# Kernel optimization log

Measured on AMD Instinct MI355X. Metric: run time of the kernel, lower is better.

The kernel has to match this reference:

```python
import jax, jax.numpy as jnp
import numpy as np

MIN_NORM = 1e-15
BALL_EPS = 1e-5  # proj margin, c = 1
HYPER_BETA = 1.0


def _artanh(x):
    x = jnp.clip(x, -1.0 + 1e-7, 1.0 - 1e-7)
    return jnp.arctanh(x)


def _proj(x):
    # clip points inside the unit Poincare ball
    norm = jnp.maximum(jnp.linalg.norm(x, axis=-1, keepdims=True), MIN_NORM)
    maxnorm = 1.0 - BALL_EPS
    return jnp.where(norm > maxnorm, x / norm * maxnorm, x)


def _expmap0(u):
    un = jnp.maximum(jnp.linalg.norm(u, axis=-1, keepdims=True), MIN_NORM)
    return jnp.tanh(un) * u / un


def _mobius_add(x, y):
    x2 = jnp.sum(x * x, axis=-1, keepdims=True)
    y2 = jnp.sum(y * y, axis=-1, keepdims=True)
    xy = jnp.sum(x * y, axis=-1, keepdims=True)
    num = (1.0 + 2.0 * xy + y2) * x + (1.0 - x2) * y
    den = 1.0 + 2.0 * xy + x2 * y2
    return num / jnp.maximum(den, MIN_NORM)


def _sqdist(p, q):
    ma = _mobius_add(-p, q)
    d = 2.0 * _artanh(jnp.linalg.norm(ma, axis=-1))
    return d * d


def _to_klein(x):
    return 2.0 * x / (1.0 + jnp.sum(x * x, axis=-1, keepdims=True))


def _lorentz_factor(x):
    return 1.0 / jnp.sqrt(jnp.maximum(1.0 - jnp.sum(x * x, axis=-1), 1e-7))


def _klein_to(x):
    return x / (1.0 + jnp.sqrt(jnp.maximum(1.0 - jnp.sum(x * x, axis=-1, keepdims=True), 0.0)))


def _logmap0(p):
    pn = jnp.maximum(jnp.linalg.norm(p, axis=-1, keepdims=True), MIN_NORM)
    return _artanh(pn) * p / pn


def setup_inputs() -> dict:
    key = jax.random.key(0)
    k1, k2, k3, k4, k5 = jax.random.split(key, 5)
    B, L, V, D, A, S = 4096, 50, 50000, 200, 14, 30
    inputs = jax.random.randint(k1, (B, L), 0, V, dtype=jnp.int32)
    emb = jax.random.normal(k2, (V, D), dtype=jnp.float32) * 0.1  # w2v * 0.1 as in student_init
    xav = float(np.sqrt(6.0 / (D + D)))
    M = jax.random.uniform(k3, (D, D), dtype=jnp.float32, minval=-xav, maxval=xav)
    a_emb = jax.random.normal(k4, (A, S, D), dtype=jnp.float32) * 0.1
    sw = jax.random.uniform(k5, (A, S), dtype=jnp.float32)
    seed_w = sw / jnp.sum(jnp.abs(sw), axis=1, keepdims=True)  # L1-normalized
    return {"inputs": inputs, "emb": emb, "M": M, "a_emb": a_emb, "seed_w": seed_w}


def reference(inputs, emb, M, a_emb, seed_w):
    # --- AttentionEncoder ---
    x_wrd = emb[inputs]                                   # [B,L,D] gather
    x_avg = jnp.mean(x_wrd, axis=1)                       # [B,D]
    scores = jnp.einsum('bld,de,be->bl', x_wrd, M, x_avg)  # [B,L]
    a = jax.nn.softmax(scores, axis=1)
    enc = jnp.einsum('bl,bld->bd', a, x_wrd)              # [B,D]

    # --- hyperbolic projection ---
    enc = _proj(_expmap0(enc))                            # [B,D] on Poincare ball
    a_emb_w = jnp.sum(a_emb * seed_w[:, :, None], axis=1)  # [A,D]
    hyp_a = _proj(_expmap0(a_emb_w))                      # [A,D]

    sqd = _sqdist(enc[:, None, :], hyp_a[None, :, :])     # [B,A]
    probs_exp = jnp.exp(-HYPER_BETA * sqd - 0.05)         # [B,A]
    a_probs = probs_exp / jnp.sum(probs_exp, axis=1, keepdims=True)

    kle = _to_klein(hyp_a)                                # [A,D]
    lf = _lorentz_factor(kle)                             # [A]
    probs = lf[None, :] * probs_exp                       # [B,A]
    probs_expanded = (probs / jnp.sum(probs, axis=1, keepdims=True))[:, :, None]  # [B,A,1]

    kle_o = jnp.sum(kle[None, :, :] * probs_expanded, axis=1)  # [B,D] Klein barycenter
    r = _klein_to(kle_o)                                  # [B,D]
    eu_r = _logmap0(r)                                    # [B,D]
    return eu_r, probs_expanded, a_probs
```

## Files before the change

### kernel.cpp

```cpp
#include <hip/hip_runtime.h>
#include <hip/hip_fp16.h>
#include <math.h>

#define B_ 4096
#define L_ 50
#define D_ 200
#define A_ 14
#define S_ 30

#define WS_HYP   0
#define WS_KLE   (A_ * D_)
#define WS_Y2    (2 * A_ * D_)
#define WS_LF    (WS_Y2 + A_)
#define WS_MH    8192
#define WS_V     8192

__device__ __forceinline__ float wave_reduce_sum(float v) {
    #pragma unroll
    for (int off = 32; off > 0; off >>= 1) v += __shfl_down(v, off, 64);
    return v;
}
__device__ __forceinline__ float bfly_sum(float v) {
    #pragma unroll
    for (int m = 32; m > 0; m >>= 1) v += __shfl_xor(v, m, 64);
    return v;
}
__device__ __forceinline__ float bfly_sum16(float v) {
    #pragma unroll
    for (int m = 8; m > 0; m >>= 1) v += __shfl_xor(v, m, 64);
    return v;
}
__device__ __forceinline__ float block_reduce_512(float val, volatile float* red) {
    __syncthreads();
    val = wave_reduce_sum(val);
    if ((threadIdx.x & 63) == 0) red[threadIdx.x >> 6] = val;
    __syncthreads();
    float s = 0.f;
    #pragma unroll
    for (int i = 0; i < 8; ++i) s += red[i];
    return s;
}

typedef _Float16 h2v __attribute__((ext_vector_type(2)));
__device__ __forceinline__ float fd2(unsigned a, unsigned b, float c) {
#if __has_builtin(__builtin_amdgcn_fdot2)
    return __builtin_amdgcn_fdot2(__builtin_bit_cast(h2v, a),
                                  __builtin_bit_cast(h2v, b), c, false);
#else
    __half2 ha = __builtin_bit_cast(__half2, a), hb = __builtin_bit_cast(__half2, b);
    float2 fa = __half22float2(ha), fb = __half22float2(hb);
    return fmaf(fa.x, fb.x, fmaf(fa.y, fb.y, c));
#endif
}
__device__ __forceinline__ unsigned packh2(float a, float b) {
    __half2 h = __floats2half2_rn(a, b);
    return __builtin_bit_cast(unsigned, h);
}

__global__ __launch_bounds__(256) void precompute_anchors(
    const float* __restrict__ a_emb, const float* __restrict__ seed_w,
    float* __restrict__ ws)
{
    __shared__ float u[A_][D_];
    __shared__ float nrm2[A_];
    const int t = threadIdx.x;
    const int wave = t >> 6, lane = t & 63;

    for (int d = t; d < D_; d += 256) {
        for (int a = 0; a < A_; ++a) {
            float acc = 0.f;
            #pragma unroll 5
            for (int s = 0; s < S_; ++s)
                acc += a_emb[(a * S_ + s) * D_ + d] * seed_w[a * S_ + s];
            u[a][d] = acc;
        }
    }
    __syncthreads();

    for (int a = wave; a < A_; a += 4) {
        float s = 0.f;
        for (int d = lane; d < D_; d += 64) s += u[a][d] * u[a][d];
        s = wave_reduce_sum(s);
        if (lane == 0) nrm2[a] = s;
    }
    __syncthreads();

    float* hyp = ws + WS_HYP;
    float* kle = ws + WS_KLE;
    float* y2  = ws + WS_Y2;
    float* lf  = ws + WS_LF;
    const float maxn = 1.0f - 1e-5f;

    for (int a = 0; a < A_; ++a) {
        float un = fmaxf(sqrtf(nrm2[a]), 1e-15f);
        float th = tanhf(un);
        float pn = fminf(th, maxn);
        float s  = pn / un;
        float py2 = pn * pn;
        float kscale = 2.0f / (1.0f + py2);
        float k2 = py2 * kscale * kscale;
        if (t == 0) {
            y2[a] = py2;
            lf[a] = 1.0f / sqrtf(fmaxf(1.0f - k2, 1e-7f));
        }
        for (int d = t; d < D_; d += 256) {
            float h = u[a][d] * s;
            hyp[a * D_ + d] = h;
            kle[a * D_ + d] = h * kscale;
        }
    }
}

__global__ __launch_bounds__(256) void convert_M(
    const float* __restrict__ M, __half* __restrict__ Mh)
{
    int i = blockIdx.x * 256 + threadIdx.x;
    if (i < D_ * D_) Mh[i] = __float2half(M[i]);
}

__global__ __launch_bounds__(256, 6) void fused_wave2(
    const int*   __restrict__ inputs,
    const float* __restrict__ emb,
    const float* __restrict__ ws,
    float* __restrict__ out)
{
    __shared__ float xav[2][2][D_];
    __shared__ float vsh[2][D_];
    __shared__ float ench[2][2][D_];
    __shared__ float msh[2][2][2];

    const float*  kle = ws + WS_KLE;
    const float*  y2  = ws + WS_Y2;
    const float*  lf  = ws + WS_LF;
    const __half* Mh  = (const __half*)(ws + WS_MH);

    const int wid  = threadIdx.x >> 6, lane = threadIdx.x & 63;
    const int rib  = wid >> 1;
    const int h    = wid & 1;
    const int b    = blockIdx.x * 2 + rib;
    const bool L50 = (lane < 50);

    const int sidx = inputs[b * L_ + (L50 ? lane : 0)];
    const int off  = L50 ? 4 * lane : 0;
    const int lbase = 25 * h;

    float a0 = 0.f, a1 = 0.f, a2 = 0.f, a3 = 0.f;
    #pragma unroll 5
    for (int j = 0; j < 25; ++j) {
        const int row = __shfl(sidx, lbase + j, 64);
        float4 x = *(const float4*)(emb + (size_t)row * D_ + off);
        a0 += x.x; a1 += x.y; a2 += x.z; a3 += x.w;
    }
    if (L50) {
        xav[rib][h][4 * lane + 0] = a0;
        xav[rib][h][4 * lane + 1] = a1;
        xav[rib][h][4 * lane + 2] = a2;
        xav[rib][h][4 * lane + 3] = a3;
    }
    __syncthreads();
    unsigned xu0 = 0, xu1 = 0;
    if (L50) {
        const float inv = 1.0f / (float)L_;
        float f0 = (xav[rib][0][4 * lane + 0] + xav[rib][1][4 * lane + 0]) * inv;
        float f1 = (xav[rib][0][4 * lane + 1] + xav[rib][1][4 * lane + 1]) * inv;
        float f2 = (xav[rib][0][4 * lane + 2] + xav[rib][1][4 * lane + 2]) * inv;
        float f3 = (xav[rib][0][4 * lane + 3] + xav[rib][1][4 * lane + 3]) * inv;
        xu0 = packh2(f0, f1);
        xu1 = packh2(f2, f3);
    }

    {
        float w0 = 0.f, w1 = 0.f;
        const int mr = 100 * h + 2 * (L50 ? lane : 0);
        const __half* m0 = Mh + (size_t)(mr + 0) * D_;
        const __half* m1 = Mh + (size_t)(mr + 1) * D_;
        #pragma unroll 5
        for (int c = 0; c < 25; ++c) {
            unsigned xa = __shfl(xu0, 2 * c,     64);
            unsigned xb = __shfl(xu1, 2 * c,     64);
            unsigned xc = __shfl(xu0, 2 * c + 1, 64);
            unsigned xd = __shfl(xu1, 2 * c + 1, 64);
            uint4 q0 = *(const uint4*)(m0 + 8 * c);
            uint4 q1 = *(const uint4*)(m1 + 8 * c);
            w0 = fd2(q0.x, xa, w0); w0 = fd2(q0.y, xb, w0); w0 = fd2(q0.z, xc, w0); w0 = fd2(q0.w, xd, w0);
            w1 = fd2(q1.x, xa, w1); w1 = fd2(q1.y, xb, w1); w1 = fd2(q1.z, xc, w1); w1 = fd2(q1.w, xd, w1);
        }
        if (L50) { vsh[rib][mr] = w0; vsh[rib][mr + 1] = w1; }
    }
    __syncthreads();
    float v0 = 0.f, v1 = 0.f, v2 = 0.f, v3 = 0.f;
    if (L50) {
        v0 = vsh[rib][4 * lane + 0];
        v1 = vsh[rib][4 * lane + 1];
        v2 = vsh[rib][4 * lane + 2];
        v3 = vsh[rib][4 * lane + 3];
    }

    float m = -INFINITY, ssum = 0.f;
    float e0 = 0.f, e1 = 0.f, e2 = 0.f, e3 = 0.f;
    {
        float4 bufA[5], bufB[5];
        auto LOADC = [&](float4* xb, int base) {
            #pragma unroll
            for (int j = 0; j < 5; ++j) {
                const int r = __shfl(sidx, lbase + base + j, 64);
                xb[j] = *(const float4*)(emb + (size_t)r * D_ + off);
            }
        };
        auto PROC = [&](const float4* xb) {
            #pragma unroll
            for (int j = 0; j < 5; ++j) {
                const float4 x = xb[j];
                float part = L50 ? (x.x * v0 + x.y * v1 + x.z * v2 + x.w * v3) : 0.f;
                const float s = bfly_sum(part);
                if (s > m) {
                    const float r = expf(m - s);
                    ssum *= r; e0 *= r; e1 *= r; e2 *= r; e3 *= r;
                    m = s;
                }
                const float w = expf(s - m);
                ssum += w;
                e0 = fmaf(w, x.x, e0); e1 = fmaf(w, x.y, e1);
                e2 = fmaf(w, x.z, e2); e3 = fmaf(w, x.w, e3);
            }
        };
        LOADC(bufA, 0);
        LOADC(bufB, 5);  PROC(bufA);
        LOADC(bufA, 10); PROC(bufB);
        LOADC(bufB, 15); PROC(bufA);
        LOADC(bufA, 20); PROC(bufB);
        PROC(bufA);
    }
    if (L50) {
        ench[rib][h][4 * lane + 0] = e0;
        ench[rib][h][4 * lane + 1] = e1;
        ench[rib][h][4 * lane + 2] = e2;
        ench[rib][h][4 * lane + 3] = e3;
    }
    if (lane == 0) { msh[rib][h][0] = m; msh[rib][h][1] = ssum; }
    __syncthreads();

    {
        const float mo  = msh[rib][1 - h][0];
        const float sso = msh[rib][1 - h][1];
        const float M   = fmaxf(m, mo);
        const float wA  = expf(m - M);
        const float wB  = expf(mo - M);
        const float st  = ssum * wA + sso * wB;
        const float rs  = 1.0f / st;
        if (L50) {
            e0 = (e0 * wA + ench[rib][1 - h][4 * lane + 0] * wB) * rs;
            e1 = (e1 * wA + ench[rib][1 - h][4 * lane + 1] * wB) * rs;
            e2 = (e2 * wA + ench[rib][1 - h][4 * lane + 2] * wB) * rs;
            e3 = (e3 * wA + ench[rib][1 - h][4 * lane + 3] * wB) * rs;
        } else {
            e0 = e1 = e2 = e3 = 0.f;
        }
    }

    const float n2 = bfly_sum(e0 * e0 + e1 * e1 + e2 * e2 + e3 * e3);
    const float un = fmaxf(sqrtf(n2), 1e-15f);
    const float pn = fminf(tanhf(un), 1.0f - 1e-5f);
    const float ps = pn / un;
    const float x2 = pn * pn;
    const float p0 = e0 * ps, p1 = e1 * ps, p2 = e2 * ps, p3 = e3 * ps;

    float kd = 0.f;
    #pragma unroll
    for (int a = 0; a < A_; ++a) {
        float4 k = *(const float4*)(kle + a * D_ + off);
        float part = L50 ? (p0 * k.x + p1 * k.y + p2 * k.z + p3 * k.w) : 0.f;
        float d = bfly_sum(part);
        if (lane == a) kd = d;
    }

    float px = 0.f, lfv = 0.f;
    if (lane < A_) {
        const float yy  = y2[lane];
        lfv = lf[lane];
        const float dot = kd * (1.0f + yy) * 0.5f;
        const float c1 = 1.0f - 2.0f * dot + yy;
        const float c2 = 1.0f - x2;
        const float num2 = c1 * c1 * x2 - 2.0f * c1 * c2 * dot + c2 * c2 * yy;
        const float den  = fmaxf(1.0f - 2.0f * dot + x2 * yy, 1e-15f);
        const float nma  = sqrtf(fmaxf(num2, 0.f)) / den;
        const float z    = fminf(nma, 1.0f - 1e-7f);
        const float dist = logf((1.0f + z) / (1.0f - z));
        px = expf(-dist * dist - 0.05f);
    }
    const float se = bfly_sum16(px);
    const float sp = bfly_sum16(lfv * px);
    float pev = 0.f;
    if (lane < A_) {
        pev = lfv * px / sp;
        if (h == 0) {
            out[B_ * D_ + b * A_ + lane] = pev;
            out[B_ * D_ + B_ * A_ + b * A_ + lane] = px / se;
        }
    }

    float k0 = 0.f, k1 = 0.f, k2 = 0.f, k3 = 0.f;
    #pragma unroll
    for (int a = 0; a < A_; ++a) {
        const float w = __shfl(pev, a, 64);
        float4 k = *(const float4*)(kle + a * D_ + off);
        k0 = fmaf(w, k.x, k0); k1 = fmaf(w, k.y, k1);
        k2 = fmaf(w, k.z, k2); k3 = fmaf(w, k.w, k3);
    }
    if (!L50) { k0 = k1 = k2 = k3 = 0.f; }
    const float n2k = bfly_sum(k0 * k0 + k1 * k1 + k2 * k2 + k3 * k3);
    const float denom = 1.0f + sqrtf(fmaxf(1.0f - n2k, 0.f));
    const float r2 = n2k / (denom * denom);
    const float rn = fmaxf(sqrtf(r2), 1e-15f);
    const float z2 = fminf(rn, 1.0f - 1e-7f);
    const float fac = 0.5f * logf((1.0f + z2) / (1.0f - z2)) / rn;
    if (L50 && h == 0) {
        float4 o = make_float4(fac * k0 / denom, fac * k1 / denom,
                               fac * k2 / denom, fac * k3 / denom);
        *(float4*)(out + (size_t)b * D_ + 4 * lane) = o;
    }
}

#define G_R 8
__global__ __launch_bounds__(512) void gather_gemm(
    const int* __restrict__ inputs, const float* __restrict__ emb,
    const float* __restrict__ M, float* __restrict__ ws)
{
    __shared__ __align__(16) float xs[G_R][D_ + 4];
    __shared__ int sidx[G_R][L_];
    float* v = ws + WS_V;
    const int b0 = blockIdx.x * G_R;
    const int t = threadIdx.x;
    const int wave = t >> 6, lane = t & 63;

    for (int p = t; p < G_R * L_; p += 512) sidx[p / L_][p % L_] = inputs[b0 * L_ + p];
    __syncthreads();

    if (lane < D_ / 4) {
        float ax = 0.f, ay = 0.f, az = 0.f, aw = 0.f;
        #pragma unroll
        for (int l = 0; l < L_; ++l) {
            const float4 vv = ((const float4*)(emb + (size_t)sidx[wave][l] * D_))[lane];
            ax += vv.x; ay += vv.y; az += vv.z; aw += vv.w;
        }
        const float inv = 1.0f / (float)L_;
        ((float4*)xs[wave])[lane] = make_float4(ax * inv, ay * inv, az * inv, aw * inv);
    }
    __syncthreads();

    const int r = t & 7, dg = t >> 3;
    const float4* xr4 = (const float4*)xs[r];
    #pragma unroll
    for (int k = 0; k < 4; ++k) {
        const int d = dg + 64 * k;
        if (d < D_) {
            const float4* Mr4 = (const float4*)(M + d * D_);
            float acc = 0.f;
            #pragma unroll
            for (int e = 0; e < D_ / 4; ++e) {
                float4 m4 = Mr4[e], x4 = xr4[e];
                acc += m4.x * x4.x + m4.y * x4.y + m4.z * x4.z + m4.w * x4.w;
            }
            v[(size_t)(b0 + r) * D_ + d] = acc;
        }
    }
}

__global__ __launch_bounds__(512, 8) void fused_main(
    const int*   __restrict__ inputs,
    const float* __restrict__ emb,
    const float* __restrict__ ws,
    float* __restrict__ out)
{
    __shared__ __align__(16) float x[L_][D_];
    __shared__ float attn[L_];
    __shared__ int   sidx[L_];
    __shared__ float red[8];
    __shared__ float sums[2];

    const float* hyp = ws + WS_HYP;
    const float* kle = ws + WS_KLE;
    const float* y2  = ws + WS_Y2;
    const float* lf  = ws + WS_LF;
    const float* vg  = ws + WS_V;

    const int b = blockIdx.x;
    const int t = threadIdx.x;
    const int wave = t >> 6, lane = t & 63;

    float vr0 = vg[(size_t)b * D_ + lane];
    float vr1 = vg[(size_t)b * D_ + lane + 64];
    float vr2 = vg[(size_t)b * D_ + lane + 128];
    float vr3 = (lane < D_ - 192) ? vg[(size_t)b * D_ + lane + 192] : 0.f;

    if (t < L_) sidx[t] = inputs[b * L_ + t];
    __syncthreads();

    {
        const int DQ = D_ / 4;
        const int p0 = t, p1 = t + 512, p2 = t + 1024, p3 = t + 1536, p4 = t + 2048;
        const bool has4 = (p4 < L_ * DQ);
        float4 a0 = ((const float4*)(emb + (size_t)sidx[p0 / DQ] * D_))[p0 % DQ];
        float4 a1 = ((const float4*)(emb + (size_t)sidx[p1 / DQ] * D_))[p1 % DQ];
        float4 a2 = ((const float4*)(emb + (size_t)sidx[p2 / DQ] * D_))[p2 % DQ];
        float4 a3 = ((const float4*)(emb + (size_t)sidx[p3 / DQ] * D_))[p3 % DQ];
        float4 a4;
        if (has4) a4 = ((const float4*)(emb + (size_t)sidx[p4 / DQ] * D_))[p4 % DQ];
        ((float4*)x[p0 / DQ])[p0 % DQ] = a0;
        ((float4*)x[p1 / DQ])[p1 % DQ] = a1;
        ((float4*)x[p2 / DQ])[p2 % DQ] = a2;
        ((float4*)x[p3 / DQ])[p3 % DQ] = a3;
        if (has4) ((float4*)x[p4 / DQ])[p4 % DQ] = a4;
    }
    __syncthreads();

    for (int l = wave; l < L_; l += 8) {
        float s = x[l][lane] * vr0 + x[l][lane + 64] * vr1 + x[l][lane + 128] * vr2;
        if (lane < D_ - 192) s += x[l][lane + 192] * vr3;
        s = wave_reduce_sum(s);
        if (lane == 0) attn[l] = s;
    }
    __syncthreads();

    if (wave == 0) {
        float scv = (lane < L_) ? attn[lane] : -INFINITY;
        float m = scv;
        #pragma unroll
        for (int off = 32; off > 0; off >>= 1) m = fmaxf(m, __shfl_xor(m, off, 64));
        float e = (lane < L_) ? expf(scv - m) : 0.f;
        float ss = e;
        #pragma unroll
        for (int off = 32; off > 0; off >>= 1) ss += __shfl_xor(ss, off, 64);
        if (lane < L_) attn[lane] = e / ss;
    }
    __syncthreads();

    float encv = 0.f;
    if (t < D_) {
        #pragma unroll 10
        for (int l = 0; l < L_; ++l) encv += attn[l] * x[l][t];
    }

    float n2 = block_reduce_512((t < D_) ? encv * encv : 0.f, red);
    const float maxn = 1.0f - 1e-5f;
    float un = fmaxf(sqrtf(n2), 1e-15f);
    float pn = fminf(tanhf(un), maxn);
    float ps = pn / un;
    float x2 = pn * pn;
    float* pvec  = &x[0][0];
    float* dotpq = &x[1][0];
    float* pexp  = &x[1][16];
    float* pe    = &x[1][32];
    if (t < D_) pvec[t] = encv * ps;
    __syncthreads();

    for (int a = wave; a < A_; a += 8) {
        const float* ha = hyp + a * D_;
        float s = ha[lane] * pvec[lane] + ha[lane + 64] * pvec[lane + 64]
                + ha[lane + 128] * pvec[lane + 128];
        if (lane < D_ - 192) s += ha[lane + 192] * pvec[lane + 192];
        s = wave_reduce_sum(s);
        if (lane == 0) dotpq[a] = s;
    }
    __syncthreads();

    if (t < A_) {
        float dot = dotpq[t];
        float yy  = y2[t];
        float c1 = 1.0f - 2.0f * dot + yy;
        float c2 = 1.0f - x2;
        float num2 = c1 * c1 * x2 - 2.0f * c1 * c2 * dot + c2 * c2 * yy;
        float den  = fmaxf(1.0f - 2.0f * dot + x2 * yy, 1e-15f);
        float nma  = sqrtf(fmaxf(num2, 0.f)) / den;
        float z    = fminf(nma, 1.0f - 1e-7f);
        float dist = logf((1.0f + z) / (1.0f - z));
        pexp[t] = expf(-dist * dist - 0.05f);
    }
    __syncthreads();
    if (t == 0) {
        float se = 0.f, sp = 0.f;
        for (int a = 0; a < A_; ++a) { se += pexp[a]; sp += lf[a] * pexp[a]; }
        sums[0] = 1.0f / se;
        sums[1] = 1.0f / sp;
    }
    __syncthreads();
    if (t < A_) {
        float ap  = pexp[t] * sums[0];
        float pev = lf[t] * pexp[t] * sums[1];
        pe[t] = pev;
        out[B_ * D_ + b * A_ + t] = pev;
        out[B_ * D_ + B_ * A_ + b * A_ + t] = ap;
    }
    __syncthreads();

    float ko = 0.f;
    if (t < D_) {
        #pragma unroll
        for (int a = 0; a < A_; ++a) ko += kle[a * D_ + t] * pe[a];
    }
    float n2k = block_reduce_512((t < D_) ? ko * ko : 0.f, red);
    if (t < D_) {
        float denom = 1.0f + sqrtf(fmaxf(1.0f - n2k, 0.f));
        float rv = ko / denom;
        float r2 = n2k / (denom * denom);
        float rn = fmaxf(sqrtf(r2), 1e-15f);
        float z  = fminf(rn, 1.0f - 1e-7f);
        float fac = (0.5f * logf((1.0f + z) / (1.0f - z))) / rn;
        out[b * D_ + t] = fac * rv;
    }
}

extern "C" void kernel_launch(void* const* d_in, const int* in_sizes, int n_in,
                              void* d_out, int out_size, void* d_ws, size_t ws_size,
                              hipStream_t stream) {
    (void)in_sizes; (void)n_in; (void)out_size;
    const int*   inputs = (const int*)  d_in[0];
    const float* emb    = (const float*)d_in[1];
    const float* M      = (const float*)d_in[2];
    const float* a_emb  = (const float*)d_in[3];
    const float* seed_w = (const float*)d_in[4];
    float* out = (float*)d_out;
    float* ws  = (float*)d_ws;

    precompute_anchors<<<1, 256, 0, stream>>>(a_emb, seed_w, ws);

    const size_t need = (size_t)(WS_MH + (D_ * D_ + 1) / 2) * sizeof(float);
    if (ws_size >= need) {
        __half* Mh = (__half*)(ws + WS_MH);
        convert_M<<<(D_ * D_ + 255) / 256, 256, 0, stream>>>(M, Mh);
        fused_wave2<<<B_ / 2, 256, 0, stream>>>(inputs, emb, ws, out);
    } else {
        gather_gemm<<<B_ / G_R, 512, 0, stream>>>(inputs, emb, M, ws);
        fused_main<<<B_, 512, 0, stream>>>(inputs, emb, ws, out);
    }
}
```

Before: 111.2 us.

## Convert embedding table to fp16 and cache gathered rows in registers

Adds a per-call pass that converts the whole 50000x200 embedding table to half precision in workspace. A new fused kernel then gathers half rows, keeps the 25 gathered rows per wave in registers, and reuses them for the mean, the scores and the weighted sum, replacing repeated global reloads. The conversion pass reads 40MB and writes 20MB on every call, which may cost more than the gather traffic it saves. Embeddings are also rounded to fp16, which adds numerical error.

```diff
diff --git a/kernel.cpp b/kernel.cpp
--- a/kernel.cpp
+++ b/kernel.cpp
@@ -13,6 +13,8 @@
 #define WS_Y2    (2 * A_ * D_)
 #define WS_LF    (WS_Y2 + A_)
 #define WS_MH    8192
+#define WS_EMBH  (WS_MH + 20000)
+#define EMBH_FLOATS ((50000 * D_) / 2)
 #define WS_V     8192
 
 __device__ __forceinline__ float wave_reduce_sum(float v) {
@@ -23,6 +25,11 @@
 __device__ __forceinline__ float bfly_sum(float v) {
     #pragma unroll
     for (int m = 32; m > 0; m >>= 1) v += __shfl_xor(v, m, 64);
+    return v;
+}
+__device__ __forceinline__ float bfly_max(float v) {
+    #pragma unroll
+    for (int m = 32; m > 0; m >>= 1) v = fmaxf(v, __shfl_xor(v, m, 64));
     return v;
 }
 __device__ __forceinline__ float bfly_sum16(float v) {
@@ -118,6 +125,209 @@
     if (i < D_ * D_) Mh[i] = __float2half(M[i]);
 }
 
+__global__ __launch_bounds__(256) void convert_emb(
+    const float* __restrict__ emb, __half* __restrict__ embh)
+{
+    const int n4 = (50000 * D_) / 4;
+    for (int i = blockIdx.x * 256 + threadIdx.x; i < n4; i += gridDim.x * 256) {
+        float4 v = ((const float4*)emb)[i];
+        uint2 u;
+        u.x = packh2(v.x, v.y);
+        u.y = packh2(v.z, v.w);
+        ((uint2*)embh)[i] = u;
+    }
+}
+
+__global__ __launch_bounds__(256, 4) void fused_wave2_h(
+    const int*   __restrict__ inputs,
+    const float* __restrict__ ws,
+    float* __restrict__ out)
+{
+    __shared__ float xav[2][2][D_];
+    __shared__ float vsh[2][D_];
+    __shared__ float ench[2][2][D_];
+    __shared__ float scoresh[2][64];
+
+    const float*  kle  = ws + WS_KLE;
+    const float*  y2   = ws + WS_Y2;
+    const float*  lf   = ws + WS_LF;
+    const __half* Mh   = (const __half*)(ws + WS_MH);
+    const __half* embh = (const __half*)(ws + WS_EMBH);
+
+    const int wid  = threadIdx.x >> 6, lane = threadIdx.x & 63;
+    const int rib  = wid >> 1;
+    const int h    = wid & 1;
+    const int b    = blockIdx.x * 2 + rib;
+    const bool L50 = (lane < 50);
+
+    const int sidx = inputs[b * L_ + (L50 ? lane : 0)];
+    const int offh = L50 ? 4 * lane : 0;
+    const int lbase = 25 * h;
+
+    uint2 tile[25];
+    float a0 = 0.f, a1 = 0.f, a2 = 0.f, a3 = 0.f;
+    #pragma unroll
+    for (int j = 0; j < 25; ++j) {
+        const int row = __shfl(sidx, lbase + j, 64);
+        uint2 u = *(const uint2*)(embh + (size_t)row * D_ + offh);
+        tile[j] = u;
+        float2 f0 = __half22float2(__builtin_bit_cast(__half2, u.x));
+        float2 f1 = __half22float2(__builtin_bit_cast(__half2, u.y));
+        a0 += f0.x; a1 += f0.y; a2 += f1.x; a3 += f1.y;
+    }
+    if (L50) {
+        xav[rib][h][4 * lane + 0] = a0;
+        xav[rib][h][4 * lane + 1] = a1;
+        xav[rib][h][4 * lane + 2] = a2;
+        xav[rib][h][4 * lane + 3] = a3;
+    }
+    __syncthreads();
+
+    unsigned xu0 = 0, xu1 = 0;
+    if (L50) {
+        const float inv = 1.0f / (float)L_;
+        float f0 = (xav[rib][0][4*lane+0] + xav[rib][1][4*lane+0]) * inv;
+        float f1 = (xav[rib][0][4*lane+1] + xav[rib][1][4*lane+1]) * inv;
+        float f2 = (xav[rib][0][4*lane+2] + xav[rib][1][4*lane+2]) * inv;
+        float f3 = (xav[rib][0][4*lane+3] + xav[rib][1][4*lane+3]) * inv;
+        xu0 = packh2(f0, f1);
+        xu1 = packh2(f2, f3);
+    }
+
+    {
+        float w0 = 0.f, w1 = 0.f;
+        const int mr = 100 * h + 2 * (L50 ? lane : 0);
+        const __half* m0 = Mh + (size_t)(mr + 0) * D_;
+        const __half* m1 = Mh + (size_t)(mr + 1) * D_;
+        #pragma unroll 5
+        for (int c = 0; c < 25; ++c) {
+            unsigned xa = __shfl(xu0, 2 * c,     64);
+            unsigned xb = __shfl(xu1, 2 * c,     64);
+            unsigned xc = __shfl(xu0, 2 * c + 1, 64);
+            unsigned xd = __shfl(xu1, 2 * c + 1, 64);
+            uint4 q0 = *(const uint4*)(m0 + 8 * c);
+            uint4 q1 = *(const uint4*)(m1 + 8 * c);
+            w0 = fd2(q0.x, xa, w0); w0 = fd2(q0.y, xb, w0); w0 = fd2(q0.z, xc, w0); w0 = fd2(q0.w, xd, w0);
+            w1 = fd2(q1.x, xa, w1); w1 = fd2(q1.y, xb, w1); w1 = fd2(q1.z, xc, w1); w1 = fd2(q1.w, xd, w1);
+        }
+        if (L50) { vsh[rib][mr] = w0; vsh[rib][mr + 1] = w1; }
+    }
+    __syncthreads();
+    float v0 = 0.f, v1 = 0.f, v2 = 0.f, v3 = 0.f;
+    if (L50) {
+        v0 = vsh[rib][4 * lane + 0];
+        v1 = vsh[rib][4 * lane + 1];
+        v2 = vsh[rib][4 * lane + 2];
+        v3 = vsh[rib][4 * lane + 3];
+    }
+
+    #pragma unroll
+    for (int j = 0; j < 25; ++j) {
+        const uint2 u = tile[j];
+        float2 f0 = __half22float2(__builtin_bit_cast(__half2, u.x));
+        float2 f1 = __half22float2(__builtin_bit_cast(__half2, u.y));
+        float part = L50 ? (f0.x * v0 + f0.y * v1 + f1.x * v2 + f1.y * v3) : 0.f;
+        const float s = bfly_sum(part);
+        if (lane == 0) scoresh[rib][lbase + j] = s;
+    }
+    __syncthreads();
+
+    const float sv = L50 ? scoresh[rib][lane] : -INFINITY;
+    const float mx = bfly_max(sv);
+    const float ex = L50 ? expf(sv - mx) : 0.f;
+    const float sm = bfly_sum(ex);
+    const float attnv = ex / sm;
+
+    float e0 = 0.f, e1 = 0.f, e2 = 0.f, e3 = 0.f;
+    #pragma unroll
+    for (int j = 0; j < 25; ++j) {
+        const float wl = __shfl(attnv, lbase + j, 64);
+        const uint2 u = tile[j];
+        float2 f0 = __half22float2(__builtin_bit_cast(__half2, u.x));
+        float2 f1 = __half22float2(__builtin_bit_cast(__half2, u.y));
+        e0 = fmaf(wl, f0.x, e0); e1 = fmaf(wl, f0.y, e1);
+        e2 = fmaf(wl, f1.x, e2); e3 = fmaf(wl, f1.y, e3);
+    }
+    if (L50) {
+        ench[rib][h][4 * lane + 0] = e0;
+        ench[rib][h][4 * lane + 1] = e1;
+        ench[rib][h][4 * lane + 2] = e2;
+        ench[rib][h][4 * lane + 3] = e3;
+    }
+    __syncthreads();
+    if (L50) {
+        e0 = ench[rib][0][4*lane+0] + ench[rib][1][4*lane+0];
+        e1 = ench[rib][0][4*lane+1] + ench[rib][1][4*lane+1];
+        e2 = ench[rib][0][4*lane+2] + ench[rib][1][4*lane+2];
+        e3 = ench[rib][0][4*lane+3] + ench[rib][1][4*lane+3];
+    } else {
+        e0 = e1 = e2 = e3 = 0.f;
+    }
+
+    const float n2 = bfly_sum(e0 * e0 + e1 * e1 + e2 * e2 + e3 * e3);
+    const float un = fmaxf(sqrtf(n2), 1e-15f);
+    const float pn = fminf(tanhf(un), 1.0f - 1e-5f);
+    const float ps = pn / un;
+    const float x2 = pn * pn;
+    const float p0 = e0 * ps, p1 = e1 * ps, p2 = e2 * ps, p3 = e3 * ps;
+    const int off = L50 ? 4 * lane : 0;
+
+    float kd = 0.f;
+    #pragma unroll
+    for (int a = 0; a < A_; ++a) {
+        float4 k = *(const float4*)(kle + a * D_ + off);
+        float part = L50 ? (p0 * k.x + p1 * k.y + p2 * k.z + p3 * k.w) : 0.f;
+        float d = bfly_sum(part);
+        if (lane == a) kd = d;
+    }
+
+    float px = 0.f, lfv = 0.f;
+    if (lane < A_) {
+        const float yy  = y2[lane];
+        lfv = lf[lane];
+        const float dot = kd * (1.0f + yy) * 0.5f;
+        const float c1 = 1.0f - 2.0f * dot + yy;
+        const float c2 = 1.0f - x2;
+        const float num2 = c1 * c1 * x2 - 2.0f * c1 * c2 * dot + c2 * c2 * yy;
+        const float den  = fmaxf(1.0f - 2.0f * dot + x2 * yy, 1e-15f);
+        const float nma  = sqrtf(fmaxf(num2, 0.f)) / den;
+        const float z    = fminf(nma, 1.0f - 1e-7f);
+        const float dist = logf((1.0f + z) / (1.0f - z));
+        px = expf(-dist * dist - 0.05f);
+    }
+    const float se = bfly_sum16(px);
+    const float sp = bfly_sum16(lfv * px);
+    float pev = 0.f;
+    if (lane < A_) {
+        pev = lfv * px / sp;
+        if (h == 0) {
+            out[B_ * D_ + b * A_ + lane] = pev;
+            out[B_ * D_ + B_ * A_ + b * A_ + lane] = px / se;
+        }
+    }
+
+    float k0 = 0.f, k1 = 0.f, k2 = 0.f, k3 = 0.f;
+    #pragma unroll
+    for (int a = 0; a < A_; ++a) {
+        const float w = __shfl(pev, a, 64);
+        float4 k = *(const float4*)(kle + a * D_ + off);
+        k0 = fmaf(w, k.x, k0); k1 = fmaf(w, k.y, k1);
+        k2 = fmaf(w, k.z, k2); k3 = fmaf(w, k.w, k3);
+    }
+    if (!L50) { k0 = k1 = k2 = k3 = 0.f; }
+    const float n2k = bfly_sum(k0 * k0 + k1 * k1 + k2 * k2 + k3 * k3);
+    const float denom = 1.0f + sqrtf(fmaxf(1.0f - n2k, 0.f));
+    const float r2 = n2k / (denom * denom);
+    const float rn = fmaxf(sqrtf(r2), 1e-15f);
+    const float z2 = fminf(rn, 1.0f - 1e-7f);
+    const float fac = 0.5f * logf((1.0f + z2) / (1.0f - z2)) / rn;
+    if (L50 && h == 0) {
+        float4 o = make_float4(fac * k0 / denom, fac * k1 / denom,
+                               fac * k2 / denom, fac * k3 / denom);
+        *(float4*)(out + (size_t)b * D_ + 4 * lane) = o;
+    }
+}
+
 __global__ __launch_bounds__(256, 6) void fused_wave2(
     const int*   __restrict__ inputs,
     const float* __restrict__ emb,
@@ -161,10 +371,10 @@
     unsigned xu0 = 0, xu1 = 0;
     if (L50) {
         const float inv = 1.0f / (float)L_;
-        float f0 = (xav[rib][0][4 * lane + 0] + xav[rib][1][4 * lane + 0]) * inv;
-        float f1 = (xav[rib][0][4 * lane + 1] + xav[rib][1][4 * lane + 1]) * inv;
-        float f2 = (xav[rib][0][4 * lane + 2] + xav[rib][1][4 * lane + 2]) * inv;
-        float f3 = (xav[rib][0][4 * lane + 3] + xav[rib][1][4 * lane + 3]) * inv;
+        float f0 = (xav[rib][0][4*lane+0] + xav[rib][1][4*lane+0]) * inv;
+        float f1 = (xav[rib][0][4*lane+1] + xav[rib][1][4*lane+1]) * inv;
+        float f2 = (xav[rib][0][4*lane+2] + xav[rib][1][4*lane+2]) * inv;
+        float f3 = (xav[rib][0][4*lane+3] + xav[rib][1][4*lane+3]) * inv;
         xu0 = packh2(f0, f1);
         xu1 = packh2(f2, f3);
     }
@@ -524,8 +734,15 @@
 
     precompute_anchors<<<1, 256, 0, stream>>>(a_emb, seed_w, ws);
 
-    const size_t need = (size_t)(WS_MH + (D_ * D_ + 1) / 2) * sizeof(float);
-    if (ws_size >= need) {
+    const size_t need_mh   = (size_t)(WS_MH + 20000) * sizeof(float);
+    const size_t need_embh = (size_t)(WS_EMBH + EMBH_FLOATS) * sizeof(float);
+    if (ws_size >= need_embh) {
+        __half* Mh   = (__half*)(ws + WS_MH);
+        __half* embh = (__half*)(ws + WS_EMBH);
+        convert_M<<<(D_ * D_ + 255) / 256, 256, 0, stream>>>(M, Mh);
+        convert_emb<<<2048, 256, 0, stream>>>(emb, embh);
+        fused_wave2_h<<<B_ / 2, 256, 0, stream>>>(inputs, ws, out);
+    } else if (ws_size >= need_mh) {
         __half* Mh = (__half*)(ws + WS_MH);
         convert_M<<<(D_ * D_ + 255) / 256, 256, 0, stream>>>(M, Mh);
         fused_wave2<<<B_ / 2, 256, 0, stream>>>(inputs, emb, ws, out);
```

After: 162.5 us. 46.2% more time.
